# Kernel tuning notes

Hardware: AMD Instinct MI355X
Metric: run time of the kernel (lower is better)

## Reference

```python
import jax, jax.numpy as jnp
import numpy as np

N_NODES = 50000
N_EDGES = 600000
D = 128
HEADS = 4
CH = D // HEADS  # 32 channels per head
NEG_SLOPE = 0.2


def setup_inputs() -> dict:
    key = jax.random.key(0)
    ks = jax.random.split(key, 16)
    x = jax.random.normal(ks[0], (N_NODES, D), dtype=jnp.float32)
    # edges with src != dst so that appending self-loops matches PyG's
    # remove_self_loops + add_self_loops exactly
    src = jax.random.randint(ks[1], (N_EDGES,), 0, N_NODES, dtype=jnp.int32)
    off = jax.random.randint(ks[2], (N_EDGES,), 1, N_NODES, dtype=jnp.int32)
    dst = (src + off) % N_NODES
    edge_index = jnp.stack([src, dst], axis=0)
    s = 1.0 / np.sqrt(D)
    def layer_params(k):
        k1, k2, k3, k4 = jax.random.split(k, 4)
        return (jax.random.normal(k1, (D, D), jnp.float32) * s,
                jax.random.normal(k2, (HEADS, CH), jnp.float32) * s,
                jax.random.normal(k3, (HEADS, CH), jnp.float32) * s,
                jnp.zeros((D,), jnp.float32),
                jax.random.normal(k4, (D, D), jnp.float32) * s)
    W1, att_src1, att_dst1, bias1, Wskip1 = layer_params(ks[3])
    W2, att_src2, att_dst2, bias2, Wskip2 = layer_params(ks[4])
    return dict(x=x, edge_index=edge_index,
                W1=W1, att_src1=att_src1, att_dst1=att_dst1, bias1=bias1, Wskip1=Wskip1,
                W2=W2, att_src2=att_src2, att_dst2=att_dst2, bias2=bias2, Wskip2=Wskip2)


def _gat_block(x, src, dst, W, a_src, a_dst, bias, Wskip):
    N = x.shape[0]
    h = (x @ W).reshape(N, HEADS, CH)                       # [N,H,C]
    asrc = jnp.einsum('nhc,hc->nh', h, a_src)               # [N,H]
    adst = jnp.einsum('nhc,hc->nh', h, a_dst)
    e = jax.nn.leaky_relu(asrc[src] + adst[dst], NEG_SLOPE)  # [E,H]
    m = jax.ops.segment_max(e, dst, num_segments=N)
    m = jnp.where(jnp.isfinite(m), m, 0.0)                  # guard empty segments
    e = jnp.exp(e - m[dst])
    denom = jax.ops.segment_sum(e, dst, num_segments=N)
    alpha = e / (denom[dst] + 1e-16)                        # segment softmax over dst
    msg = h[src] * alpha[:, :, None]                        # [E,H,C]
    agg = jax.ops.segment_sum(msg, dst, num_segments=N)
    out = agg.reshape(N, D) + bias + x @ Wskip              # conv + skip
    return jax.nn.elu(out)


def reference(x, edge_index, W1, att_src1, att_dst1, bias1, Wskip1,
              W2, att_src2, att_dst2, bias2, Wskip2):
    N = x.shape[0]
    loops = jnp.arange(N, dtype=edge_index.dtype)
    src = jnp.concatenate([edge_index[0], loops])
    dst = jnp.concatenate([edge_index[1], loops])
    x = _gat_block(x, src, dst, W1, att_src1, att_dst1, bias1, Wskip1)
    x = _gat_block(x, src, dst, W2, att_src2, att_dst2, bias2, Wskip2)
    return x
```

## Files before the change

kernel.cpp:

```cpp
#include <hip/hip_runtime.h>
#include <hip/hip_bf16.h>

#define NN 50000
#define NE 600000
#define DD 128
#define NH 4
#define ET (NE + NN)
#define NEG_SLOPE 0.2f

typedef __attribute__((ext_vector_type(8))) short short8;
typedef __attribute__((ext_vector_type(4))) float f32x4;

__device__ __forceinline__ float bf2f(unsigned short u) {
    union { unsigned int i; float f; } c; c.i = ((unsigned int)u) << 16; return c.f;
}
__device__ __forceinline__ unsigned short f2bf(float f) {
    union { float f; unsigned int i; } c; c.f = f;
    unsigned int r = c.i + 0x7FFF + ((c.i >> 16) & 1);
    return (unsigned short)(r >> 16);
}


__global__ void __launch_bounds__(256) prep_k(const float* __restrict__ W1, const float* __restrict__ Ws1,
                                              const float* __restrict__ W2, const float* __restrict__ Ws2,
                                              unsigned short* __restrict__ Wt, int* __restrict__ counts) {
    int idx = blockIdx.x * 256 + threadIdx.x;
    int mat = idx >> 14;
    int p = idx & 16383;
    int col = p >> 7;
    int cs = (p >> 3) & 15;
    int j = p & 7;
    int c = cs ^ (col & 7);
    int k = c * 8 + j;
    const float* Wsrc = (mat == 0) ? W1 : (mat == 1) ? Ws1 : (mat == 2) ? W2 : Ws2;
    Wt[idx] = f2bf(Wsrc[k * DD + col]);
    if (idx < NN) counts[idx] = 0;
}


__global__ void __launch_bounds__(1024) scan_k(const int* __restrict__ counts, int* __restrict__ offsets,
                                               int* __restrict__ cursor, int* __restrict__ esrc) {
    __shared__ int part[1024];
    int tid = threadIdx.x;
    const int4* c4 = (const int4*)counts;
    const int NI4 = NN / 4;
    const int CH = (NI4 + 1023) / 1024;
    int beg4 = tid * CH;
    int end4 = beg4 + CH < NI4 ? beg4 + CH : NI4;
    int s = 0;
    for (int i = beg4; i < end4; ++i) {
        int4 v = c4[i];
        s += v.x + v.y + v.z + v.w + 4;
    }
    part[tid] = s;
    __syncthreads();
    for (int off = 1; off < 1024; off <<= 1) {
        int v = (tid >= off) ? part[tid - off] : 0;
        __syncthreads();
        part[tid] += v;
        __syncthreads();
    }
    int running = part[tid] - s;
    for (int i = beg4; i < end4; ++i) {
        int4 v = c4[i];
        int node = i * 4;
        int4 o;
        o.x = running;
        o.y = o.x + v.x + 1;
        o.z = o.y + v.y + 1;
        o.w = o.z + v.z + 1;
        running = o.w + v.w + 1;
        ((int4*)offsets)[i] = o;
        ((int4*)cursor)[i] = o;
        esrc[o.x + v.x] = node;
        esrc[o.y + v.y] = node + 1;
        esrc[o.z + v.z] = node + 2;
        esrc[o.w + v.w] = node + 3;
    }
    if (tid == 0) offsets[NN] = ET;
}

__global__ void __launch_bounds__(256) scatter_k(const int* __restrict__ src, const int* __restrict__ dst,
                                                 int* __restrict__ cursor, int* __restrict__ esrc) {
    int e = blockIdx.x * 256 + threadIdx.x;
    if (e < NE) {
        int pos = atomicAdd(&cursor[dst[e]], 1);
        esrc[pos] = src[e];
    }
}


#define GGEMM ((NN + 127) / 128)

template <bool F32IN>
__global__ void __launch_bounds__(512) gemm2_k(const void* __restrict__ xin,
                                               const unsigned short* __restrict__ Wl,
                                               const float* __restrict__ a_src, const float* __restrict__ a_dst,
                                               unsigned short* __restrict__ h2, unsigned short* __restrict__ skipb,
                                               float* __restrict__ nsrc, float* __restrict__ ndst,
                                               const int* __restrict__ e_dst, int* __restrict__ counts) {
    __shared__ __align__(16) unsigned char wlds[65536];
    if (F32IN && blockIdx.x >= GGEMM) {
        int e = (blockIdx.x - GGEMM) * 512 + threadIdx.x;
        if (e < NE) atomicAdd(&counts[e_dst[e]], 1);
        return;
    }
    int row0 = blockIdx.x * 128;
    int tid = threadIdx.x;
    int w = tid >> 6, lidx = tid & 63;
    int lrow = lidx & 15, lk = lidx >> 4;
    int srow = row0 + w * 16 + lrow;
    int rclamp = srow < NN ? srow : NN - 1;

    short8 afrag[4];
    if (F32IN) {
        const float* xp = (const float*)xin + (size_t)rclamp * DD;
#pragma unroll
        for (int kc = 0; kc < 4; ++kc) {
            float4 u0 = *(const float4*)(xp + kc * 32 + lk * 8);
            float4 u1 = *(const float4*)(xp + kc * 32 + lk * 8 + 4);
            short8 a;
            a[0] = (short)f2bf(u0.x); a[1] = (short)f2bf(u0.y);
            a[2] = (short)f2bf(u0.z); a[3] = (short)f2bf(u0.w);
            a[4] = (short)f2bf(u1.x); a[5] = (short)f2bf(u1.y);
            a[6] = (short)f2bf(u1.z); a[7] = (short)f2bf(u1.w);
            afrag[kc] = a;
        }
    } else {
        const unsigned short* xp = (const unsigned short*)xin + (size_t)rclamp * DD;
#pragma unroll
        for (int kc = 0; kc < 4; ++kc)
            afrag[kc] = *(const short8*)(xp + kc * 32 + lk * 8);
    }

    {
        const uint4* g = (const uint4*)Wl;
        uint4* l = (uint4*)wlds;
#pragma unroll
        for (int i = 0; i < 8; ++i)
            l[i * 512 + tid] = g[i * 512 + tid];
    }
    __syncthreads();

    f32x4 zero = {0.f, 0.f, 0.f, 0.f};
    f32x4 acch[8], accs[8];
#pragma unroll
    for (int t = 0; t < 8; ++t) { acch[t] = zero; accs[t] = zero; }

#pragma unroll
    for (int kc = 0; kc < 4; ++kc) {
        short8 a = afrag[kc];
#pragma unroll
        for (int t = 0; t < 8; ++t) {
            int off = (t * 16 + lrow) * 256 + (((kc * 4 + lk) ^ (lrow & 7)) * 16);
            short8 b  = *(const short8*)&wlds[off];
            short8 bs = *(const short8*)&wlds[off + 32768];
            acch[t] = __builtin_amdgcn_mfma_f32_16x16x32_bf16(a, b, acch[t], 0, 0, 0);
            accs[t] = __builtin_amdgcn_mfma_f32_16x16x32_bf16(a, bs, accs[t], 0, 0, 0);
        }
    }

#pragma unroll
    for (int t = 0; t < 8; ++t) {
#pragma unroll
        for (int q = 0; q < 4; ++q) {
            int grow = row0 + w * 16 + lk * 4 + q;
            if (grow < NN) {
                int col = t * 16 + lrow;
                h2[(size_t)grow * DD + col] = f2bf(acch[t][q]);
                skipb[(size_t)grow * DD + col] = f2bf(accs[t][q]);
            }
        }
    }

    float as_lo[NH], as_hi[NH], ad_lo[NH], ad_hi[NH];
#pragma unroll
    for (int h = 0; h < NH; ++h) {
        as_lo[h] = a_src[h * 32 + lrow];
        as_hi[h] = a_src[h * 32 + 16 + lrow];
        ad_lo[h] = a_dst[h * 32 + lrow];
        ad_hi[h] = a_dst[h * 32 + 16 + lrow];
    }
#pragma unroll
    for (int h = 0; h < NH; ++h) {
#pragma unroll
        for (int q = 0; q < 4; ++q) {
            float ps = acch[2 * h][q] * as_lo[h] + acch[2 * h + 1][q] * as_hi[h];
            float pd = acch[2 * h][q] * ad_lo[h] + acch[2 * h + 1][q] * ad_hi[h];
#pragma unroll
            for (int off = 1; off < 16; off <<= 1) {
                ps += __shfl_xor(ps, off);
                pd += __shfl_xor(pd, off);
            }
            if (lrow == 0) {
                int grow = row0 + w * 16 + lk * 4 + q;
                if (grow < NN) {
                    nsrc[grow * 4 + h] = ps;
                    ndst[grow * 4 + h] = pd;
                }
            }
        }
    }
}


__global__ void __launch_bounds__(256) aggregate_k(const unsigned short* __restrict__ h2,
                                                   const unsigned short* __restrict__ skipb,
                                                   const float* __restrict__ nsrc, const float* __restrict__ ndst,
                                                   const int* __restrict__ offsets, const int* __restrict__ esrc,
                                                   const float* __restrict__ bias, float* __restrict__ outf,
                                                   unsigned short* __restrict__ outb) {
    int n = blockIdx.x * 4 + (threadIdx.x >> 6);
    int i = threadIdx.x & 63;
    int e = i & 15, hc = i >> 4;
    int gbase = i & 48;
    int beg = offsets[n], end = offsets[n + 1];
    float ad = ndst[n * 4 + hc];
    const unsigned int* h2w = (const unsigned int*)h2;

    float m = -1e30f, den = 0.f, acc0 = 0.f, acc1 = 0.f;
    for (int base = beg; base < end; base += 16) {
        int j = base + e;
        int jc = j < end ? j : end - 1;
        int s = esrc[jc];
        float a = nsrc[s * 4 + hc] + ad;
        a = a > 0.f ? a : NEG_SLOPE * a;
        if (j >= end) a = -1e30f;
        float cm = a;
        cm = fmaxf(cm, __shfl_xor(cm, 1));
        cm = fmaxf(cm, __shfl_xor(cm, 2));
        cm = fmaxf(cm, __shfl_xor(cm, 4));
        cm = fmaxf(cm, __shfl_xor(cm, 8));
        float mn = fmaxf(m, cm);
        float scale = __expf(m - mn);
        float wgt = __expf(a - mn);
        m = mn;
        float sw = wgt;
        sw += __shfl_xor(sw, 1);
        sw += __shfl_xor(sw, 2);
        sw += __shfl_xor(sw, 4);
        sw += __shfl_xor(sw, 8);
        den = den * scale + sw;
        acc0 *= scale;
        acc1 *= scale;
#pragma unroll
        for (int e2 = 0; e2 < 16; ++e2) {
            int se = __shfl(s, e2);
            float we = __shfl(wgt, gbase + e2);
            unsigned hv = h2w[se * 64 + i];
            acc0 = fmaf(we, bf2f((unsigned short)(hv & 0xFFFF)), acc0);
            acc1 = fmaf(we, bf2f((unsigned short)(hv >> 16)), acc1);
        }
    }
    float inv = 1.f / (den + 1e-16f);
    int c0 = 2 * i;
    unsigned sk = ((const unsigned int*)skipb)[n * 64 + i];
    float2 bv = *(const float2*)&bias[c0];
    float o0 = acc0 * inv + bv.x + bf2f((unsigned short)(sk & 0xFFFF));
    float o1 = acc1 * inv + bv.y + bf2f((unsigned short)(sk >> 16));
    o0 = o0 > 0.f ? o0 : expm1f(o0);
    o1 = o1 > 0.f ? o1 : expm1f(o1);
    size_t o = (size_t)n * DD;
    if (outf) { outf[o + c0] = o0; outf[o + c0 + 1] = o1; }
    if (outb) { outb[o + c0] = f2bf(o0); outb[o + c0 + 1] = f2bf(o1); }
}


extern "C" void kernel_launch(void* const* d_in, const int* in_sizes, int n_in,
                              void* d_out, int out_size, void* d_ws, size_t ws_size,
                              hipStream_t stream) {
    const float* x   = (const float*)d_in[0];
    const int* eidx  = (const int*)d_in[1];
    const float* W1  = (const float*)d_in[2];
    const float* as1 = (const float*)d_in[3];
    const float* ad1 = (const float*)d_in[4];
    const float* b1  = (const float*)d_in[5];
    const float* Ws1 = (const float*)d_in[6];
    const float* W2  = (const float*)d_in[7];
    const float* as2 = (const float*)d_in[8];
    const float* ad2 = (const float*)d_in[9];
    const float* b2  = (const float*)d_in[10];
    const float* Ws2 = (const float*)d_in[11];
    float* out = (float*)d_out;

    const int* e_src = eidx;
    const int* e_dst = eidx + NE;

    char* p = (char*)d_ws;
    unsigned short* h2    = (unsigned short*)p; p += (size_t)NN * DD * 2;
    unsigned short* xb    = (unsigned short*)p; p += (size_t)NN * DD * 2;
    unsigned short* skipb = (unsigned short*)p; p += (size_t)NN * DD * 2;
    float* nsrc = (float*)p; p += (size_t)NN * NH * 4;
    float* ndst = (float*)p; p += (size_t)NN * NH * 4;
    unsigned short* Wt = (unsigned short*)p; p += (size_t)4 * DD * DD * 2;
    int* counts  = (int*)p; p += (size_t)NN * 4;
    int* offsets = (int*)p; p += (size_t)(NN + 4) * 4;
    int* cursor  = (int*)p; p += (size_t)NN * 4;
    int* esrc    = (int*)p; p += (size_t)ET * 4;

    const int CB = (NE + 511) / 512;

    prep_k<<<256, 256, 0, stream>>>(W1, Ws1, W2, Ws2, Wt, counts);

    gemm2_k<true><<<GGEMM + CB, 512, 0, stream>>>(x, Wt, as1, ad1, h2, skipb, nsrc, ndst, e_dst, counts);

    scan_k<<<1, 1024, 0, stream>>>(counts, offsets, cursor, esrc);
    scatter_k<<<(NE + 255) / 256, 256, 0, stream>>>(e_src, e_dst, cursor, esrc);

    aggregate_k<<<NN / 4, 256, 0, stream>>>(h2, skipb, nsrc, ndst, offsets, esrc, b1, nullptr, xb);

    gemm2_k<false><<<GGEMM, 512, 0, stream>>>(xb, Wt + 32768, as2, ad2, h2, skipb, nsrc, ndst, e_dst, counts);
    aggregate_k<<<NN / 4, 256, 0, stream>>>(h2, skipb, nsrc, ndst, offsets, esrc, b2, out, nullptr);
}
```

Before: 300.5 us.

## Replace single-block prefix scan with atomic-append offset allocation

The single-workgroup scan kernel that computed CSR offsets is replaced by a grid-wide kernel where each node claims its segment with an atomicAdd on a shared tail counter. Segments are no longer in node order, so aggregate now derives each segment's end from the count instead of the next offset. Degree counting moves from the GEMM launch into the weight-prep launch, and a memset replaces the in-kernel zeroing of the counts. This removes a serial one-block step, at the cost of heavy atomic contention on one counter and scattered segment placement that may hurt locality in scatter and aggregate.

```diff
diff --git a/kernel.cpp b/kernel.cpp
--- a/kernel.cpp
+++ b/kernel.cpp
@@ -7,6 +7,7 @@
 #define NH 4
 #define ET (NE + NN)
 #define NEG_SLOPE 0.2f
+#define CBLK ((NE + 255) / 256)
 
 typedef __attribute__((ext_vector_type(8))) short short8;
 typedef __attribute__((ext_vector_type(4))) float f32x4;
@@ -23,7 +24,13 @@
 
 __global__ void __launch_bounds__(256) prep_k(const float* __restrict__ W1, const float* __restrict__ Ws1,
                                               const float* __restrict__ W2, const float* __restrict__ Ws2,
-                                              unsigned short* __restrict__ Wt, int* __restrict__ counts) {
+                                              unsigned short* __restrict__ Wt,
+                                              const int* __restrict__ e_dst, int* __restrict__ counts) {
+    if (blockIdx.x >= 256) {
+        int e = (blockIdx.x - 256) * 256 + threadIdx.x;
+        if (e < NE) atomicAdd(&counts[e_dst[e]], 1);
+        return;
+    }
     int idx = blockIdx.x * 256 + threadIdx.x;
     int mat = idx >> 14;
     int p = idx & 16383;
@@ -34,50 +41,20 @@
     int k = c * 8 + j;
     const float* Wsrc = (mat == 0) ? W1 : (mat == 1) ? Ws1 : (mat == 2) ? W2 : Ws2;
     Wt[idx] = f2bf(Wsrc[k * DD + col]);
-    if (idx < NN) counts[idx] = 0;
-}
-
-
-__global__ void __launch_bounds__(1024) scan_k(const int* __restrict__ counts, int* __restrict__ offsets,
-                                               int* __restrict__ cursor, int* __restrict__ esrc) {
-    __shared__ int part[1024];
-    int tid = threadIdx.x;
-    const int4* c4 = (const int4*)counts;
-    const int NI4 = NN / 4;
-    const int CH = (NI4 + 1023) / 1024;
-    int beg4 = tid * CH;
-    int end4 = beg4 + CH < NI4 ? beg4 + CH : NI4;
-    int s = 0;
-    for (int i = beg4; i < end4; ++i) {
-        int4 v = c4[i];
-        s += v.x + v.y + v.z + v.w + 4;
-    }
-    part[tid] = s;
-    __syncthreads();
-    for (int off = 1; off < 1024; off <<= 1) {
-        int v = (tid >= off) ? part[tid - off] : 0;
-        __syncthreads();
-        part[tid] += v;
-        __syncthreads();
-    }
-    int running = part[tid] - s;
-    for (int i = beg4; i < end4; ++i) {
-        int4 v = c4[i];
-        int node = i * 4;
-        int4 o;
-        o.x = running;
-        o.y = o.x + v.x + 1;
-        o.z = o.y + v.y + 1;
-        o.w = o.z + v.z + 1;
-        running = o.w + v.w + 1;
-        ((int4*)offsets)[i] = o;
-        ((int4*)cursor)[i] = o;
-        esrc[o.x + v.x] = node;
-        esrc[o.y + v.y] = node + 1;
-        esrc[o.z + v.z] = node + 2;
-        esrc[o.w + v.w] = node + 3;
-    }
-    if (tid == 0) offsets[NN] = ET;
+}
+
+
+__global__ void __launch_bounds__(256) offsets2_k(const int* __restrict__ counts, int* __restrict__ tail,
+                                                  int* __restrict__ offsets, int* __restrict__ cursor,
+                                                  int* __restrict__ esrc) {
+    int t = blockIdx.x * 256 + threadIdx.x;
+    if (t < NN) {
+        int cnt = counts[t] + 1;
+        int beg = atomicAdd(tail, cnt);
+        offsets[t] = beg;
+        cursor[t] = beg;
+        esrc[beg + cnt - 1] = t;
+    }
 }
 
 __global__ void __launch_bounds__(256) scatter_k(const int* __restrict__ src, const int* __restrict__ dst,
@@ -97,14 +74,8 @@
                                                const unsigned short* __restrict__ Wl,
                                                const float* __restrict__ a_src, const float* __restrict__ a_dst,
                                                unsigned short* __restrict__ h2, unsigned short* __restrict__ skipb,
-                                               float* __restrict__ nsrc, float* __restrict__ ndst,
-                                               const int* __restrict__ e_dst, int* __restrict__ counts) {
+                                               float* __restrict__ nsrc, float* __restrict__ ndst) {
     __shared__ __align__(16) unsigned char wlds[65536];
-    if (F32IN && blockIdx.x >= GGEMM) {
-        int e = (blockIdx.x - GGEMM) * 512 + threadIdx.x;
-        if (e < NE) atomicAdd(&counts[e_dst[e]], 1);
-        return;
-    }
     int row0 = blockIdx.x * 128;
     int tid = threadIdx.x;
     int w = tid >> 6, lidx = tid & 63;
@@ -207,14 +178,16 @@
 __global__ void __launch_bounds__(256) aggregate_k(const unsigned short* __restrict__ h2,
                                                    const unsigned short* __restrict__ skipb,
                                                    const float* __restrict__ nsrc, const float* __restrict__ ndst,
-                                                   const int* __restrict__ offsets, const int* __restrict__ esrc,
+                                                   const int* __restrict__ offsets, const int* __restrict__ counts,
+                                                   const int* __restrict__ esrc,
                                                    const float* __restrict__ bias, float* __restrict__ outf,
                                                    unsigned short* __restrict__ outb) {
     int n = blockIdx.x * 4 + (threadIdx.x >> 6);
     int i = threadIdx.x & 63;
     int e = i & 15, hc = i >> 4;
     int gbase = i & 48;
-    int beg = offsets[n], end = offsets[n + 1];
+    int beg = offsets[n];
+    int end = beg + counts[n] + 1;
     float ad = ndst[n * 4 + hc];
     const unsigned int* h2w = (const unsigned int*)h2;
 
@@ -293,22 +266,23 @@
     float* nsrc = (float*)p; p += (size_t)NN * NH * 4;
     float* ndst = (float*)p; p += (size_t)NN * NH * 4;
     unsigned short* Wt = (unsigned short*)p; p += (size_t)4 * DD * DD * 2;
-    int* counts  = (int*)p; p += (size_t)NN * 4;
-    int* offsets = (int*)p; p += (size_t)(NN + 4) * 4;
+    int* counts  = (int*)p; p += (size_t)(NN + 1) * 4;
+    int* offsets = (int*)p; p += (size_t)NN * 4;
     int* cursor  = (int*)p; p += (size_t)NN * 4;
     int* esrc    = (int*)p; p += (size_t)ET * 4;
 
-    const int CB = (NE + 511) / 512;
-
-    prep_k<<<256, 256, 0, stream>>>(W1, Ws1, W2, Ws2, Wt, counts);
-
-    gemm2_k<true><<<GGEMM + CB, 512, 0, stream>>>(x, Wt, as1, ad1, h2, skipb, nsrc, ndst, e_dst, counts);
-
-    scan_k<<<1, 1024, 0, stream>>>(counts, offsets, cursor, esrc);
+    int* tail = counts + NN;
+
+    hipMemsetAsync(counts, 0, (size_t)(NN + 1) * 4, stream);
+
+    prep_k<<<256 + CBLK, 256, 0, stream>>>(W1, Ws1, W2, Ws2, Wt, e_dst, counts);
+
+    offsets2_k<<<(NN + 255) / 256, 256, 0, stream>>>(counts, tail, offsets, cursor, esrc);
     scatter_k<<<(NE + 255) / 256, 256, 0, stream>>>(e_src, e_dst, cursor, esrc);
 
-    aggregate_k<<<NN / 4, 256, 0, stream>>>(h2, skipb, nsrc, ndst, offsets, esrc, b1, nullptr, xb);
-
-    gemm2_k<false><<<GGEMM, 512, 0, stream>>>(xb, Wt + 32768, as2, ad2, h2, skipb, nsrc, ndst, e_dst, counts);
-    aggregate_k<<<NN / 4, 256, 0, stream>>>(h2, skipb, nsrc, ndst, offsets, esrc, b2, out, nullptr);
-}
+    gemm2_k<true><<<GGEMM, 512, 0, stream>>>(x, Wt, as1, ad1, h2, skipb, nsrc, ndst);
+    aggregate_k<<<NN / 4, 256, 0, stream>>>(h2, skipb, nsrc, ndst, offsets, counts, esrc, b1, nullptr, xb);
+
+    gemm2_k<false><<<GGEMM, 512, 0, stream>>>(xb, Wt + 32768, as2, ad2, h2, skipb, nsrc, ndst);
+    aggregate_k<<<NN / 4, 256, 0, stream>>>(h2, skipb, nsrc, ndst, offsets, counts, esrc, b2, out, nullptr);
+}
```

Result: faster. 273.9 us (-8.9%).
